# Kernel tuning notes

Measured on AMD Instinct MI355X. Metric: run time of the kernel, lower is better.

Reference implementation:

```python
import jax, jax.numpy as jnp
import numpy as np

N = 50000      # nodes
E = 800000     # edges
P = 200000     # link pairs
D_IN = 128     # input_dim
F_NUM = 128    # filter_num
OUT = 2        # out_dim
K = 10         # APPNP propagation steps
ALPHA = 0.1    # teleport prob


def setup_inputs() -> dict:
    key = jax.random.key(0)
    ks = jax.random.split(key, 9)
    x = jax.random.normal(ks[0], (N, D_IN), dtype=jnp.float32)
    edge_index = jax.random.randint(ks[1], (2, E), 0, N)
    index = jax.random.randint(ks[2], (P, 2), 0, N)
    s1 = 1.0 / np.sqrt(D_IN)
    s2 = 1.0 / np.sqrt(F_NUM)
    s3 = 1.0 / np.sqrt(2 * F_NUM)
    W1 = jax.random.uniform(ks[3], (F_NUM, D_IN), minval=-s1, maxval=s1)
    b1 = jax.random.uniform(ks[4], (F_NUM,), minval=-s1, maxval=s1)
    W2 = jax.random.uniform(ks[5], (F_NUM, F_NUM), minval=-s2, maxval=s2)
    b2 = jax.random.uniform(ks[6], (F_NUM,), minval=-s2, maxval=s2)
    W3 = jax.random.uniform(ks[7], (OUT, 2 * F_NUM), minval=-s3, maxval=s3)
    b3 = jax.random.uniform(ks[8], (OUT,), minval=-s3, maxval=s3)
    return {"x": x, "edge_index": edge_index, "index": index,
            "W1": W1, "b1": b1, "W2": W2, "b2": b2, "W3": W3, "b3": b3}


def _gcn_norm(edge_index, num_nodes):
    # PyG gcn_norm: add self-loops, sym norm D^{-1/2} (A+I) D^{-1/2}
    src, dst = edge_index[0], edge_index[1]
    loop = jnp.arange(num_nodes, dtype=src.dtype)
    src = jnp.concatenate([src, loop])
    dst = jnp.concatenate([dst, loop])
    deg = jax.ops.segment_sum(jnp.ones_like(src, dtype=jnp.float32), dst,
                              num_segments=num_nodes)
    dinv = jnp.where(deg > 0, jax.lax.rsqrt(deg), 0.0)
    norm = dinv[src] * dinv[dst]  # [E+N]
    return src, dst, norm


def _appnp(x, src, dst, norm, num_nodes):
    # h_{k+1} = (1-alpha) * A_hat h_k + alpha * x0
    def step(h, _):
        agg = jax.ops.segment_sum(norm[:, None] * h[src], dst,
                                  num_segments=num_nodes)
        return (1.0 - ALPHA) * agg + ALPHA * x, None
    h, _ = jax.lax.scan(step, x, None, length=K)
    return h


def reference(x, edge_index, index, W1, b1, W2, b2, W3, b3):
    num_nodes = x.shape[0]
    src, dst, norm = _gcn_norm(edge_index, num_nodes)
    h = x @ W1.T + b1                      # [N, F]
    h = jax.nn.relu(_appnp(h, src, dst, norm, num_nodes))
    h = h @ W2.T + b2                      # [N, F]
    h = jax.nn.relu(_appnp(h, src, dst, norm, num_nodes))
    feat = jnp.concatenate([h[index[:, 0]], h[index[:, 1]]], axis=-1)  # [P, 2F]
    out = feat @ W3.T + b3                 # [P, OUT]
    return jax.nn.log_softmax(out, axis=1)
```

## Files before the change

### kernel.cpp

```cpp
#include <hip/hip_runtime.h>
#include <math.h>

#define NN 50000
#define NE 800000
#define NP 200000
#define NF 128
#define NEDGE_TOT (NE + NN)
#define NBLK 196
#define NBK 64
#define DPB 782
#define BKCAP 16384
#define EPB 2048

typedef __attribute__((ext_vector_type(8))) short short8;
typedef __attribute__((ext_vector_type(4))) float float4v;
typedef __attribute__((ext_vector_type(2))) _Float16 h2;

__device__ __forceinline__ float bf_lo(unsigned u) { return __uint_as_float(u << 16); }
__device__ __forceinline__ float bf_hi(unsigned u) { return __uint_as_float(u & 0xffff0000u); }
__device__ __forceinline__ unsigned short f2bf(float f) {
    unsigned u = __float_as_uint(f);
    return (unsigned short)((u + 0x7fffu + ((u >> 16) & 1u)) >> 16);
}
__device__ __forceinline__ unsigned pack2bf(float a, float b) {
    return (unsigned)f2bf(a) | ((unsigned)f2bf(b) << 16);
}

__device__ __forceinline__ h2 u2h2(unsigned u) {
    union { unsigned u; h2 h; } c; c.u = u; return c.h;
}
__device__ __forceinline__ unsigned h22u(h2 h) {
    union { unsigned u; h2 h; } c; c.h = h; return c.u;
}
__device__ __forceinline__ float h_lo(unsigned u) { return (float)u2h2(u).x; }
__device__ __forceinline__ float h_hi(unsigned u) { return (float)u2h2(u).y; }
__device__ __forceinline__ unsigned pack2h(float a, float b) {
    h2 h; h.x = (_Float16)a; h.y = (_Float16)b; return h22u(h);
}

__global__ __launch_bounds__(256) void init_cnt_k(int* __restrict__ cnt) {
    int i = blockIdx.x * 256 + threadIdx.x;
    if (i < NN) cnt[i] = 1;
}

__global__ __launch_bounds__(256) void count_k(const int* __restrict__ ei,
                                               int* __restrict__ cnt) {
    int e = blockIdx.x * 256 + threadIdx.x;
    if (e < NE) atomicAdd(&cnt[ei[NE + e]], 1);
}

__global__ __launch_bounds__(256) void scan_reduce_k(const int* __restrict__ cnt,
                                                     int* __restrict__ bsum,
                                                     float* __restrict__ dinv) {
    __shared__ int s[256];
    int t = threadIdx.x;
    int idx = blockIdx.x * 256 + t;
    int v = (idx < NN) ? cnt[idx] : 0;
    if (idx < NN) dinv[idx] = rsqrtf((float)v);
    s[t] = v;
    __syncthreads();
    for (int off = 128; off > 0; off >>= 1) {
        if (t < off) s[t] += s[t + off];
        __syncthreads();
    }
    if (t == 0) bsum[blockIdx.x] = s[0];
}

__global__ __launch_bounds__(256) void scan_bsums_k(const int* __restrict__ bsum,
                                                    int* __restrict__ boff) {
    __shared__ int s[256];
    int t = threadIdx.x;
    int v = (t < NBLK) ? bsum[t] : 0;
    s[t] = v;
    __syncthreads();
    for (int off = 1; off < 256; off <<= 1) {
        int add = (t >= off) ? s[t - off] : 0;
        __syncthreads();
        s[t] += add;
        __syncthreads();
    }
    if (t < NBLK) boff[t] = s[t] - v;
}

__global__ __launch_bounds__(256) void scan_down_k(const int* __restrict__ cnt,
                                                   const int* __restrict__ boff,
                                                   int* __restrict__ row_ptr) {
    __shared__ int s[256];
    int t = threadIdx.x;
    int idx = blockIdx.x * 256 + t;
    int v = (idx < NN) ? cnt[idx] : 0;
    s[t] = v;
    __syncthreads();
    for (int off = 1; off < 256; off <<= 1) {
        int add = (t >= off) ? s[t - off] : 0;
        __syncthreads();
        s[t] += add;
        __syncthreads();
    }
    int excl = s[t] - v + boff[blockIdx.x];
    if (idx < NN) {
        row_ptr[idx] = excl;
        if (idx == NN - 1) row_ptr[NN] = excl + v;
    }
}

__global__ __launch_bounds__(256) void bin_k(const int* __restrict__ ei,
                                             int* __restrict__ gtail,
                                             int2* __restrict__ gbk) {
    __shared__ int cntA[NBK], baseA[NBK], gposA[NBK];
    __shared__ int2 stage[EPB];
    int tid = threadIdx.x;
    int ebase = blockIdx.x * EPB;
    int sv[8], dv[8], lp8[8], bk8[8];
    bool val[8];
    if (tid < NBK) cntA[tid] = 0;
    __syncthreads();
#pragma unroll
    for (int k = 0; k < 8; ++k) {
        int e = ebase + k * 256 + tid;
        val[k] = (e < NEDGE_TOT);
        if (val[k]) {
            int s, d;
            if (e < NE) { s = ei[e]; d = ei[NE + e]; }
            else        { s = d = e - NE; }
            sv[k] = s; dv[k] = d;
            bk8[k] = d / DPB;
            lp8[k] = atomicAdd(&cntA[bk8[k]], 1);
        }
    }
    __syncthreads();
    if (tid == 0) {
        int run = 0;
        for (int b = 0; b < NBK; ++b) { baseA[b] = run; run += cntA[b]; }
    }
    __syncthreads();
    if (tid < NBK && cntA[tid] > 0)
        gposA[tid] = atomicAdd(&gtail[tid], cntA[tid]);
    __syncthreads();
#pragma unroll
    for (int k = 0; k < 8; ++k)
        if (val[k]) {
            int2 r; r.x = sv[k]; r.y = dv[k];
            stage[baseA[bk8[k]] + lp8[k]] = r;
        }
    __syncthreads();
    int total = baseA[NBK - 1] + cntA[NBK - 1];
    for (int i = tid; i < total; i += 256) {
        int2 r = stage[i];
        int b = r.y / DPB;
        gbk[(size_t)b * BKCAP + gposA[b] + (i - baseA[b])] = r;
    }
}

__global__ __launch_bounds__(256) void build_k(const int* __restrict__ row_ptr,
                                               const int* __restrict__ gtail,
                                               const int2* __restrict__ gbk,
                                               int* __restrict__ cols) {
    __shared__ int wcur[DPB];
    int tid = threadIdx.x;
    int b = blockIdx.x;
    int d0 = b * DPB;
    for (int i = tid; i < DPB; i += 256) {
        int d = d0 + i;
        wcur[i] = (d < NN) ? row_ptr[d] : 0;
    }
    __syncthreads();
    int nb = gtail[b];
    const int2* src = gbk + (size_t)b * BKCAP;
    for (int t = tid; t < nb; t += 256) {
        int2 r = src[t];
        int pos = atomicAdd(&wcur[r.y - d0], 1);
        cols[pos] = r.x;
    }
}

__global__ __launch_bounds__(256) void zero_k(unsigned short* Ys1, unsigned short* Ys2,
                                              unsigned short* HA, unsigned short* HB,
                                              int* gtail) {
    int t = threadIdx.x;
    unsigned short* bufs[4] = {Ys1, Ys2, HA, HB};
    unsigned short* b = bufs[t >> 6];
    ((unsigned*)(b + (size_t)NN * NF))[t & 63] = 0u;
    if (t < NBK) gtail[t] = 0;
}

__global__ __launch_bounds__(256) void cast_w_k(const float* __restrict__ W,
                                                unsigned short* __restrict__ Wb) {
    int t = blockIdx.x * 256 + threadIdx.x;
    if (t >= 128 * 128 / 8) return;
    int i = t * 8;
    float4 f0 = *(const float4*)(W + i);
    float4 f1 = *(const float4*)(W + i + 4);
    uint4 q;
    q.x = pack2bf(f0.x, f0.y);
    q.y = pack2bf(f0.z, f0.w);
    q.z = pack2bf(f1.x, f1.y);
    q.w = pack2bf(f1.z, f1.w);
    *(uint4*)(Wb + i) = q;
}

#define GPAD 136
template <bool F32IN>
__global__ __launch_bounds__(256) void gemm_mfma_k(const void* __restrict__ Xv,
                                                   const unsigned short* __restrict__ Wb,
                                                   const float* __restrict__ bias,
                                                   const float* __restrict__ dinv,
                                                   unsigned short* __restrict__ Yu,
                                                   unsigned short* __restrict__ Ys,
                                                   int nrows) {
    __shared__ unsigned short sm[4 * 16 * GPAD];
    int wave = threadIdx.x >> 6, lane = threadIdx.x & 63;
    int rbase = blockIdx.x * 64 + wave * 16;
    if (rbase >= nrows) return;
    int quad = lane >> 4, mn = lane & 15;
    float4v acc[8];
#pragma unroll
    for (int ft = 0; ft < 8; ++ft) acc[ft] = (float4v){0.f, 0.f, 0.f, 0.f};
#pragma unroll
    for (int kb = 0; kb < 128; kb += 32) {
        short8 a;
        if (F32IN) {
            const float* X = (const float*)Xv;
            float4 f0 = *(const float4*)(X + (size_t)(rbase + mn) * NF + kb + quad * 8);
            float4 f1 = *(const float4*)(X + (size_t)(rbase + mn) * NF + kb + quad * 8 + 4);
            a[0] = (short)f2bf(f0.x); a[1] = (short)f2bf(f0.y);
            a[2] = (short)f2bf(f0.z); a[3] = (short)f2bf(f0.w);
            a[4] = (short)f2bf(f1.x); a[5] = (short)f2bf(f1.y);
            a[6] = (short)f2bf(f1.z); a[7] = (short)f2bf(f1.w);
        } else {
            const unsigned short* X = (const unsigned short*)Xv;
            a = *(const short8*)(X + (size_t)(rbase + mn) * NF + kb + quad * 8);
        }
#pragma unroll
        for (int ft = 0; ft < 8; ++ft) {
            short8 b = *(const short8*)(Wb + (size_t)(ft * 16 + mn) * NF + kb + quad * 8);
            acc[ft] = __builtin_amdgcn_mfma_f32_16x16x32_bf16(a, b, acc[ft], 0, 0, 0);
        }
    }
    unsigned short* smw = sm + wave * 16 * GPAD;
#pragma unroll
    for (int ft = 0; ft < 8; ++ft) {
        float bv = bias[ft * 16 + mn];
#pragma unroll
        for (int r = 0; r < 4; ++r) {
            union { _Float16 h; unsigned short s; } cv;
            cv.h = (_Float16)(acc[ft][r] + bv);
            smw[(quad * 4 + r) * GPAD + ft * 16 + mn] = cv.s;
        }
    }
    __syncthreads();
#pragma unroll
    for (int t = 0; t < 4; ++t) {
        int rl = t * 4 + quad;
        int row = rbase + rl;
        uint4 q = *(const uint4*)(smw + rl * GPAD + mn * 8);
        *(uint4*)(Yu + (size_t)row * NF + mn * 8) = q;
        float g = dinv[row];
        uint4 qs;
        qs.x = pack2h(g * h_lo(q.x), g * h_hi(q.x));
        qs.y = pack2h(g * h_lo(q.y), g * h_hi(q.y));
        qs.z = pack2h(g * h_lo(q.z), g * h_hi(q.z));
        qs.w = pack2h(g * h_lo(q.w), g * h_hi(q.w));
        *(uint4*)(Ys + (size_t)row * NF + mn * 8) = qs;
    }
}

__global__ __launch_bounds__(256) void appnp_h_k(const unsigned short* __restrict__ hs,
                                                 const unsigned short* __restrict__ x0,
                                                 const float* __restrict__ dinv,
                                                 unsigned short* __restrict__ out,
                                                 const int* __restrict__ row_ptr,
                                                 const int* __restrict__ cols,
                                                 int mode,
                                                 const float* __restrict__ W3,
                                                 float4* __restrict__ puv) {
    int wid = (blockIdx.x * 256 + threadIdx.x) >> 6;
    int lane = threadIdx.x & 63;
    if (wid >= NN) return;
    int half = lane >> 5, li = lane & 31;
    int beg = row_ptr[wid], end = row_ptr[wid + 1];
    h2 a01; a01.x = (_Float16)0.f; a01.y = (_Float16)0.f;
    h2 a23 = a01;
    for (int e = beg; e < end; e += 64) {
        int m = end - e;
        if (m > 64) m = 64;
        int c = (lane < m) ? cols[e + lane] : NN;
        for (int j = 0; j < m; j += 8) {
            int c0 = __shfl(c, j + half, 64);
            int c1 = __shfl(c, j + 2 + half, 64);
            int c2 = __shfl(c, j + 4 + half, 64);
            int c3 = __shfl(c, j + 6 + half, 64);
            uint2 q0 = *((const uint2*)(hs + (size_t)c0 * NF) + li);
            uint2 q1 = *((const uint2*)(hs + (size_t)c1 * NF) + li);
            uint2 q2 = *((const uint2*)(hs + (size_t)c2 * NF) + li);
            uint2 q3 = *((const uint2*)(hs + (size_t)c3 * NF) + li);
            a01 += (u2h2(q0.x) + u2h2(q1.x)) + (u2h2(q2.x) + u2h2(q3.x));
            a23 += (u2h2(q0.y) + u2h2(q1.y)) + (u2h2(q2.y) + u2h2(q3.y));
        }
    }
    a01 += u2h2((unsigned)__shfl_xor((int)h22u(a01), 32, 64));
    a23 += u2h2((unsigned)__shfl_xor((int)h22u(a23), 32, 64));
    if (half != 0) return;
    float g = dinv[wid];
    float s9 = 0.9f * g;
    uint2 xq = *((const uint2*)(x0 + (size_t)wid * NF) + li);
    float h0 = s9 * (float)a01.x + 0.1f * h_lo(xq.x);
    float h1 = s9 * (float)a01.y + 0.1f * h_hi(xq.x);
    float h2v = s9 * (float)a23.x + 0.1f * h_lo(xq.y);
    float h3 = s9 * (float)a23.y + 0.1f * h_hi(xq.y);
    if (mode == 0) {
        uint2 oq;
        oq.x = pack2h(g * h0, g * h1);
        oq.y = pack2h(g * h2v, g * h3);
        *((uint2*)(out + (size_t)wid * NF) + li) = oq;
    } else {
        h0 = fmaxf(h0, 0.f); h1 = fmaxf(h1, 0.f);
        h2v = fmaxf(h2v, 0.f); h3 = fmaxf(h3, 0.f);
        if (mode == 1) {
            uint2 oq;
            oq.x = pack2bf(h0, h1);
            oq.y = pack2bf(h2v, h3);
            *((uint2*)(out + (size_t)wid * NF) + li) = oq;
        } else {
            int fb = li * 4;
            float4 wu0 = *(const float4*)(W3 + fb);
            float4 wv0 = *(const float4*)(W3 + 128 + fb);
            float4 wu1 = *(const float4*)(W3 + 256 + fb);
            float4 wv1 = *(const float4*)(W3 + 384 + fb);
            float du0 = h0 * wu0.x + h1 * wu0.y + h2v * wu0.z + h3 * wu0.w;
            float du1 = h0 * wu1.x + h1 * wu1.y + h2v * wu1.z + h3 * wu1.w;
            float dv0 = h0 * wv0.x + h1 * wv0.y + h2v * wv0.z + h3 * wv0.w;
            float dv1 = h0 * wv1.x + h1 * wv1.y + h2v * wv1.z + h3 * wv1.w;
#pragma unroll
            for (int off = 1; off < 32; off <<= 1) {
                du0 += __shfl_xor(du0, off, 64);
                du1 += __shfl_xor(du1, off, 64);
                dv0 += __shfl_xor(dv0, off, 64);
                dv1 += __shfl_xor(dv1, off, 64);
            }
            if (li == 0) puv[wid] = make_float4(du0, du1, dv0, dv1);
        }
    }
}

__global__ __launch_bounds__(256) void pair2_k(const float4* __restrict__ puv,
                                               const int2* __restrict__ index,
                                               const float* __restrict__ b3,
                                               float* __restrict__ outp) {
    int p = blockIdx.x * 256 + threadIdx.x;
    if (p >= NP) return;
    int2 uv = index[p];
    float4 a = puv[uv.x];
    float4 b = puv[uv.y];
    float s0 = a.x + b.z + b3[0];
    float s1 = a.y + b.w + b3[1];
    float m = fmaxf(s0, s1);
    float lse = m + logf(expf(s0 - m) + expf(s1 - m));
    *(float2*)(outp + (size_t)p * 2) = make_float2(s0 - lse, s1 - lse);
}

extern "C" void kernel_launch(void* const* d_in, const int* in_sizes, int n_in,
                              void* d_out, int out_size, void* d_ws, size_t ws_size,
                              hipStream_t stream) {
    const float* x  = (const float*)d_in[0];
    const int* ei   = (const int*)d_in[1];
    const int* idx  = (const int*)d_in[2];
    const float* W1 = (const float*)d_in[3];
    const float* b1 = (const float*)d_in[4];
    const float* W2 = (const float*)d_in[5];
    const float* b2 = (const float*)d_in[6];
    const float* W3 = (const float*)d_in[7];
    const float* b3 = (const float*)d_in[8];
    float* out = (float*)d_out;

    char* ws = (char*)d_ws;
    size_t off = 0;
    auto alloc = [&](size_t bytes) -> void* {
        void* p = ws + off;
        off = (off + bytes + 255) & ~(size_t)255;
        return p;
    };
    const size_t HROWS = (size_t)(NN + 1) * NF;
    int*   cnt     = (int*)  alloc(NN * sizeof(int));
    float* dinv    = (float*)alloc(NN * sizeof(float));
    int*   row_ptr = (int*)  alloc((NN + 1) * sizeof(int));
    int*   bsum    = (int*)  alloc(NBLK * sizeof(int));
    int*   boff    = (int*)  alloc(NBLK * sizeof(int));
    int*   gtail   = (int*)  alloc(NBK * sizeof(int));
    int2*  gbk     = (int2*) alloc((size_t)NBK * BKCAP * sizeof(int2));
    int*   cols    = (int*)  alloc((size_t)NEDGE_TOT * sizeof(int));
    float4* puv    = (float4*)alloc((size_t)NN * sizeof(float4));
    unsigned short* Wb1 = (unsigned short*)alloc(128 * 128 * 2);
    unsigned short* Wb2 = (unsigned short*)alloc(128 * 128 * 2);
    unsigned short* Yu1 = (unsigned short*)alloc(HROWS * 2);
    unsigned short* Ys1 = (unsigned short*)alloc(HROWS * 2);
    unsigned short* Yu2 = (unsigned short*)alloc(HROWS * 2);
    unsigned short* Ys2 = (unsigned short*)alloc(HROWS * 2);
    unsigned short* HA  = (unsigned short*)alloc(HROWS * 2);
    unsigned short* HB  = (unsigned short*)alloc(HROWS * 2);
    unsigned short* Hrelu = (unsigned short*)alloc((size_t)NN * NF * 2);

    const int gN    = (NN + 255) / 256;
    const int gE    = (NE + 255) / 256;
    const int gBin  = (NEDGE_TOT + EPB - 1) / EPB;
    const int gGemm = (NN + 63) / 64;
    const int gStep = (NN * 64 + 255) / 256;
    const int gPair = (NP + 255) / 256;

    cast_w_k<<<8, 256, 0, stream>>>(W1, Wb1);
    cast_w_k<<<8, 256, 0, stream>>>(W2, Wb2);
    zero_k<<<1, 256, 0, stream>>>(Ys1, Ys2, HA, HB, gtail);
    init_cnt_k<<<gN, 256, 0, stream>>>(cnt);
    count_k<<<gE, 256, 0, stream>>>(ei, cnt);
    scan_reduce_k<<<NBLK, 256, 0, stream>>>(cnt, bsum, dinv);
    scan_bsums_k<<<1, 256, 0, stream>>>(bsum, boff);
    scan_down_k<<<NBLK, 256, 0, stream>>>(cnt, boff, row_ptr);
    bin_k<<<gBin, 256, 0, stream>>>(ei, gtail, gbk);
    build_k<<<NBK, 256, 0, stream>>>(row_ptr, gtail, gbk, cols);

    gemm_mfma_k<true><<<gGemm, 256, 0, stream>>>(x, Wb1, b1, dinv, Yu1, Ys1, NN);
    {
        const unsigned short* cur = Ys1;
        for (int k = 0; k < 10; ++k) {
            unsigned short* dst = (k == 9) ? Hrelu : ((k & 1) ? HB : HA);
            appnp_h_k<<<gStep, 256, 0, stream>>>(cur, Yu1, dinv, dst, row_ptr,
                                                 cols, (k == 9) ? 1 : 0, W3, puv);
            cur = dst;
        }
    }
    gemm_mfma_k<false><<<gGemm, 256, 0, stream>>>(Hrelu, Wb2, b2, dinv, Yu2, Ys2, NN);
    {
        const unsigned short* cur = Ys2;
        for (int k = 0; k < 10; ++k) {
            unsigned short* dst = (k & 1) ? HB : HA;
            appnp_h_k<<<gStep, 256, 0, stream>>>(cur, Yu2, dinv, dst, row_ptr,
                                                 cols, (k == 9) ? 2 : 0, W3, puv);
            cur = dst;
        }
    }
    pair2_k<<<gPair, 256, 0, stream>>>(puv, (const int2*)idx, b3, out);
}
```

Measured before the change: 829.4 us.

## Fuse ten APPNP propagation launches into one cooperative persistent kernel

Replaces the ten per-step SpMM kernel launches per APPNP layer with a single cooperative kernel of 1024 blocks that loops over the steps and uses grid.sync between them, with warps striding over nodes. The aim is to remove launch overhead and the tail gaps between the many short kernels. In exchange it adds grid-wide barriers and caps occupancy at four blocks per CU, which may reduce latency hiding for the gather-bound loads.

```diff
diff --git a/kernel.cpp b/kernel.cpp
--- a/kernel.cpp
+++ b/kernel.cpp
@@ -1,5 +1,8 @@
 #include <hip/hip_runtime.h>
+#include <hip/hip_cooperative_groups.h>
 #include <math.h>
+
+namespace cg = cooperative_groups;
 
 #define NN 50000
 #define NE 800000
@@ -11,6 +14,7 @@
 #define DPB 782
 #define BKCAP 16384
 #define EPB 2048
+#define GRID_CO 1024
 
 typedef __attribute__((ext_vector_type(8))) short short8;
 typedef __attribute__((ext_vector_type(4))) float float4v;
@@ -265,81 +269,95 @@
     }
 }
 
-__global__ __launch_bounds__(256) void appnp_h_k(const unsigned short* __restrict__ hs,
-                                                 const unsigned short* __restrict__ x0,
-                                                 const float* __restrict__ dinv,
-                                                 unsigned short* __restrict__ out,
-                                                 const int* __restrict__ row_ptr,
-                                                 const int* __restrict__ cols,
-                                                 int mode,
-                                                 const float* __restrict__ W3,
-                                                 float4* __restrict__ puv) {
-    int wid = (blockIdx.x * 256 + threadIdx.x) >> 6;
+__global__ __launch_bounds__(256, 4) void appnp_layer_k(
+    const unsigned short* __restrict__ hs0,
+    const unsigned short* __restrict__ x0,
+    const float* __restrict__ dinv,
+    unsigned short* __restrict__ bufA,
+    unsigned short* __restrict__ bufB,
+    unsigned short* __restrict__ outbf,
+    const int* __restrict__ row_ptr,
+    const int* __restrict__ cols,
+    int finalMode,
+    const float* __restrict__ W3,
+    float4* __restrict__ puv) {
+    cg::grid_group grid = cg::this_grid();
     int lane = threadIdx.x & 63;
-    if (wid >= NN) return;
     int half = lane >> 5, li = lane & 31;
-    int beg = row_ptr[wid], end = row_ptr[wid + 1];
-    h2 a01; a01.x = (_Float16)0.f; a01.y = (_Float16)0.f;
-    h2 a23 = a01;
-    for (int e = beg; e < end; e += 64) {
-        int m = end - e;
-        if (m > 64) m = 64;
-        int c = (lane < m) ? cols[e + lane] : NN;
-        for (int j = 0; j < m; j += 8) {
-            int c0 = __shfl(c, j + half, 64);
-            int c1 = __shfl(c, j + 2 + half, 64);
-            int c2 = __shfl(c, j + 4 + half, 64);
-            int c3 = __shfl(c, j + 6 + half, 64);
-            uint2 q0 = *((const uint2*)(hs + (size_t)c0 * NF) + li);
-            uint2 q1 = *((const uint2*)(hs + (size_t)c1 * NF) + li);
-            uint2 q2 = *((const uint2*)(hs + (size_t)c2 * NF) + li);
-            uint2 q3 = *((const uint2*)(hs + (size_t)c3 * NF) + li);
-            a01 += (u2h2(q0.x) + u2h2(q1.x)) + (u2h2(q2.x) + u2h2(q3.x));
-            a23 += (u2h2(q0.y) + u2h2(q1.y)) + (u2h2(q2.y) + u2h2(q3.y));
-        }
-    }
-    a01 += u2h2((unsigned)__shfl_xor((int)h22u(a01), 32, 64));
-    a23 += u2h2((unsigned)__shfl_xor((int)h22u(a23), 32, 64));
-    if (half != 0) return;
-    float g = dinv[wid];
-    float s9 = 0.9f * g;
-    uint2 xq = *((const uint2*)(x0 + (size_t)wid * NF) + li);
-    float h0 = s9 * (float)a01.x + 0.1f * h_lo(xq.x);
-    float h1 = s9 * (float)a01.y + 0.1f * h_hi(xq.x);
-    float h2v = s9 * (float)a23.x + 0.1f * h_lo(xq.y);
-    float h3 = s9 * (float)a23.y + 0.1f * h_hi(xq.y);
-    if (mode == 0) {
-        uint2 oq;
-        oq.x = pack2h(g * h0, g * h1);
-        oq.y = pack2h(g * h2v, g * h3);
-        *((uint2*)(out + (size_t)wid * NF) + li) = oq;
-    } else {
-        h0 = fmaxf(h0, 0.f); h1 = fmaxf(h1, 0.f);
-        h2v = fmaxf(h2v, 0.f); h3 = fmaxf(h3, 0.f);
-        if (mode == 1) {
-            uint2 oq;
-            oq.x = pack2bf(h0, h1);
-            oq.y = pack2bf(h2v, h3);
-            *((uint2*)(out + (size_t)wid * NF) + li) = oq;
-        } else {
-            int fb = li * 4;
-            float4 wu0 = *(const float4*)(W3 + fb);
-            float4 wv0 = *(const float4*)(W3 + 128 + fb);
-            float4 wu1 = *(const float4*)(W3 + 256 + fb);
-            float4 wv1 = *(const float4*)(W3 + 384 + fb);
-            float du0 = h0 * wu0.x + h1 * wu0.y + h2v * wu0.z + h3 * wu0.w;
-            float du1 = h0 * wu1.x + h1 * wu1.y + h2v * wu1.z + h3 * wu1.w;
-            float dv0 = h0 * wv0.x + h1 * wv0.y + h2v * wv0.z + h3 * wv0.w;
-            float dv1 = h0 * wv1.x + h1 * wv1.y + h2v * wv1.z + h3 * wv1.w;
-#pragma unroll
-            for (int off = 1; off < 32; off <<= 1) {
-                du0 += __shfl_xor(du0, off, 64);
-                du1 += __shfl_xor(du1, off, 64);
-                dv0 += __shfl_xor(dv0, off, 64);
-                dv1 += __shfl_xor(dv1, off, 64);
+    int wgid = (blockIdx.x * 256 + threadIdx.x) >> 6;
+    const int nw = GRID_CO * 4;
+    const unsigned short* cur = hs0;
+    for (int k = 0; k < 10; ++k) {
+        int mode = (k == 9) ? finalMode : 0;
+        unsigned short* dst = (k == 9) ? outbf : ((k & 1) ? bufB : bufA);
+        for (int wid = wgid; wid < NN; wid += nw) {
+            int beg = row_ptr[wid], end = row_ptr[wid + 1];
+            h2 a01; a01.x = (_Float16)0.f; a01.y = (_Float16)0.f;
+            h2 a23 = a01;
+            for (int e = beg; e < end; e += 64) {
+                int m = end - e;
+                if (m > 64) m = 64;
+                int c = (lane < m) ? cols[e + lane] : NN;
+                for (int j = 0; j < m; j += 8) {
+                    int c0 = __shfl(c, j + half, 64);
+                    int c1 = __shfl(c, j + 2 + half, 64);
+                    int c2 = __shfl(c, j + 4 + half, 64);
+                    int c3 = __shfl(c, j + 6 + half, 64);
+                    uint2 q0 = *((const uint2*)(cur + (size_t)c0 * NF) + li);
+                    uint2 q1 = *((const uint2*)(cur + (size_t)c1 * NF) + li);
+                    uint2 q2 = *((const uint2*)(cur + (size_t)c2 * NF) + li);
+                    uint2 q3 = *((const uint2*)(cur + (size_t)c3 * NF) + li);
+                    a01 += (u2h2(q0.x) + u2h2(q1.x)) + (u2h2(q2.x) + u2h2(q3.x));
+                    a23 += (u2h2(q0.y) + u2h2(q1.y)) + (u2h2(q2.y) + u2h2(q3.y));
+                }
             }
-            if (li == 0) puv[wid] = make_float4(du0, du1, dv0, dv1);
-        }
+            a01 += u2h2((unsigned)__shfl_xor((int)h22u(a01), 32, 64));
+            a23 += u2h2((unsigned)__shfl_xor((int)h22u(a23), 32, 64));
+            if (half == 0) {
+                float g = dinv[wid];
+                float s9 = 0.9f * g;
+                uint2 xq = *((const uint2*)(x0 + (size_t)wid * NF) + li);
+                float h0 = s9 * (float)a01.x + 0.1f * h_lo(xq.x);
+                float h1 = s9 * (float)a01.y + 0.1f * h_hi(xq.x);
+                float h2v = s9 * (float)a23.x + 0.1f * h_lo(xq.y);
+                float h3 = s9 * (float)a23.y + 0.1f * h_hi(xq.y);
+                if (mode == 0) {
+                    uint2 oq;
+                    oq.x = pack2h(g * h0, g * h1);
+                    oq.y = pack2h(g * h2v, g * h3);
+                    *((uint2*)(dst + (size_t)wid * NF) + li) = oq;
+                } else {
+                    h0 = fmaxf(h0, 0.f); h1 = fmaxf(h1, 0.f);
+                    h2v = fmaxf(h2v, 0.f); h3 = fmaxf(h3, 0.f);
+                    if (mode == 1) {
+                        uint2 oq;
+                        oq.x = pack2bf(h0, h1);
+                        oq.y = pack2bf(h2v, h3);
+                        *((uint2*)(dst + (size_t)wid * NF) + li) = oq;
+                    } else {
+                        int fb = li * 4;
+                        float4 wu0 = *(const float4*)(W3 + fb);
+                        float4 wv0 = *(const float4*)(W3 + 128 + fb);
+                        float4 wu1 = *(const float4*)(W3 + 256 + fb);
+                        float4 wv1 = *(const float4*)(W3 + 384 + fb);
+                        float du0 = h0 * wu0.x + h1 * wu0.y + h2v * wu0.z + h3 * wu0.w;
+                        float du1 = h0 * wu1.x + h1 * wu1.y + h2v * wu1.z + h3 * wu1.w;
+                        float dv0 = h0 * wv0.x + h1 * wv0.y + h2v * wv0.z + h3 * wv0.w;
+                        float dv1 = h0 * wv1.x + h1 * wv1.y + h2v * wv1.z + h3 * wv1.w;
+#pragma unroll
+                        for (int off = 1; off < 32; off <<= 1) {
+                            du0 += __shfl_xor(du0, off, 64);
+                            du1 += __shfl_xor(du1, off, 64);
+                            dv0 += __shfl_xor(dv0, off, 64);
+                            dv1 += __shfl_xor(dv1, off, 64);
+                        }
+                        if (li == 0) puv[wid] = make_float4(du0, du1, dv0, dv1);
+                    }
+                }
+            }
+        }
+        if (k < 9) grid.sync();
+        cur = dst;
     }
 }
 
@@ -404,7 +422,6 @@
     const int gE    = (NE + 255) / 256;
     const int gBin  = (NEDGE_TOT + EPB - 1) / EPB;
     const int gGemm = (NN + 63) / 64;
-    const int gStep = (NN * 64 + 255) / 256;
     const int gPair = (NP + 255) / 256;
 
     cast_w_k<<<8, 256, 0, stream>>>(W1, Wb1);
@@ -420,23 +437,23 @@
 
     gemm_mfma_k<true><<<gGemm, 256, 0, stream>>>(x, Wb1, b1, dinv, Yu1, Ys1, NN);
     {
-        const unsigned short* cur = Ys1;
-        for (int k = 0; k < 10; ++k) {
-            unsigned short* dst = (k == 9) ? Hrelu : ((k & 1) ? HB : HA);
-            appnp_h_k<<<gStep, 256, 0, stream>>>(cur, Yu1, dinv, dst, row_ptr,
-                                                 cols, (k == 9) ? 1 : 0, W3, puv);
-            cur = dst;
-        }
+        int fm = 1;
+        void* args[] = {(void*)&Ys1, (void*)&Yu1, (void*)&dinv,
+                        (void*)&HA, (void*)&HB, (void*)&Hrelu,
+                        (void*)&row_ptr, (void*)&cols, (void*)&fm,
+                        (void*)&W3, (void*)&puv};
+        hipLaunchCooperativeKernel((void*)appnp_layer_k, dim3(GRID_CO), dim3(256),
+                                   args, 0, stream);
     }
     gemm_mfma_k<false><<<gGemm, 256, 0, stream>>>(Hrelu, Wb2, b2, dinv, Yu2, Ys2, NN);
     {
-        const unsigned short* cur = Ys2;
-        for (int k = 0; k < 10; ++k) {
-            unsigned short* dst = (k & 1) ? HB : HA;
-            appnp_h_k<<<gStep, 256, 0, stream>>>(cur, Yu2, dinv, dst, row_ptr,
-                                                 cols, (k == 9) ? 2 : 0, W3, puv);
-            cur = dst;
-        }
+        int fm = 2;
+        void* args[] = {(void*)&Ys2, (void*)&Yu2, (void*)&dinv,
+                        (void*)&HA, (void*)&HB, (void*)&Hrelu,
+                        (void*)&row_ptr, (void*)&cols, (void*)&fm,
+                        (void*)&W3, (void*)&puv};
+        hipLaunchCooperativeKernel((void*)appnp_layer_k, dim3(GRID_CO), dim3(256),
+                                   args, 0, stream);
     }
     pair2_k<<<gPair, 256, 0, stream>>>(puv, (const int2*)idx, b3, out);
 }
```

New measurement: 3.132 ms. +277.7%, slower.
